# Performance work log

Hardware: AMD Instinct MI355X
Metric: run time of the kernel (lower is better)

The kernel has to match this reference:

```python
import jax, jax.numpy as jnp
import numpy as np

MARGIN = 0.3
NORM = 2.0  # p-norm used by both pairwise() and PairwiseDistance

M, C = 65536, 256   # n*h*w pixels, feature channels
K, P, Q = 20, 2048, 2048  # classes 1..nclass-1, positives, negatives per class


def setup_inputs() -> dict:
    key = jax.random.key(0)
    k1, k2, k3 = jax.random.split(key, 3)
    features = jax.random.normal(k1, (M, C), dtype=jnp.float32)
    pos_idx = jax.random.randint(k2, (K, P), 0, M)
    neg_idx = jax.random.randint(k3, (K, Q), 0, M)
    return {"features": features, "pos_idx": pos_idx, "neg_idx": neg_idx}


def _pairwise(x, y):
    # torch: clamp(xx - 2xy + yy, 0); (dis + eps) ** (1/norm)
    eps = 0.0001 / x.shape[1]
    xx = jnp.sum(x * x, axis=1)           # [P]
    yy = jnp.sum(y * y, axis=1)           # [Q]
    xy = x @ y.T                           # [P,Q] GEMM
    dis = jnp.clip(xx[:, None] - 2.0 * xy + yy[None, :], 0.0)
    return (dis + eps) ** (1.0 / NORM)


def _pdist(x1, x2):
    # PairwiseDistance: (clamp(sum(|x1-x2|^p), 0) + eps) ** (1/p)
    eps = 0.0001 / x1.shape[1]
    out = jnp.sum(jnp.abs(x1 - x2) ** NORM, axis=1)
    return (jnp.clip(out, 0.0) + eps) ** (1.0 / NORM)


def _class_loss(pos, neg):
    # hard mining on detached features (indices only, as in generate_triplet_simple)
    pos_d = jax.lax.stop_gradient(pos)
    neg_d = jax.lax.stop_gradient(neg)
    hp = jnp.argmax(_pairwise(pos_d, pos_d), axis=1)   # hardest positive per anchor
    hn = jnp.argmin(_pairwise(pos_d, neg_d), axis=1)   # hardest negative per anchor
    d_p = _pdist(pos, pos[hp])
    d_n = _pdist(pos, neg[hn])
    return jnp.mean(jnp.clip(MARGIN + d_p - d_n, 0.0))


def reference(features, pos_idx, neg_idx):
    f = jax.nn.sigmoid(features)          # torch.sigmoid(features)
    pos = f[pos_idx]                      # [K,P,C]
    neg = f[neg_idx]                      # [K,Q,C]
    losses = jax.vmap(_class_loss)(pos, neg)  # per-class triplet losses
    return jnp.sum(losses)                # loss accumulated over classes
```

## Files before the change

### kernel.cpp

```cpp
#include <hip/hip_runtime.h>
#include <stdint.h>

#define M_ROWS 65536
#define C_DIM  256
#define K_CLS  20
#define P_POS  2048
#define MARGIN_F 0.3f
#define EPS_D (0.0001f / 256.0f)
#define SCALE1 0x7F7F7F7Fu
#define SCALE2 0x80808080u

typedef float floatx4 __attribute__((ext_vector_type(4)));
typedef int   intx8   __attribute__((ext_vector_type(8)));
union Frag8 { intx8 v; uint4 q[2]; };

__device__ __forceinline__ void async_copy16(const void* g, void* l) {
    __builtin_amdgcn_global_load_lds(
        (const __attribute__((address_space(1))) void*)g,
        (__attribute__((address_space(3))) void*)l, 16, 0, 0);
}
__device__ __forceinline__ float sigm(float x) { return 1.f / (1.f + __expf(-x)); }

__device__ __forceinline__ void negA(Frag8& f) {
#pragma unroll
    for (int t = 0; t < 8; ++t) f.v[t] ^= (int)0x80808080u;
}

#define VMCNT2() asm volatile("s_waitcnt vmcnt(2)" ::: "memory")
#define VMCNT0() asm volatile("s_waitcnt vmcnt(0)" ::: "memory")

__global__ __launch_bounds__(256) void sigmoid_norm_k(
        const float* __restrict__ feat,
        unsigned int* __restrict__ S8,
        float* __restrict__ xx,
        unsigned int* __restrict__ hp,
        unsigned int* __restrict__ hn,
        float* __restrict__ out) {
    {
        const int idx = blockIdx.x * 256 + threadIdx.x;
        if (idx < K_CLS * P_POS) { hp[idx] = 0u; hn[idx] = 0xFFFFFFFFu; }
        if (idx == 0) out[0] = 0.f;
    }
    const int wave = threadIdx.x >> 6, lane = threadIdx.x & 63;
    for (int g = blockIdx.x; g < M_ROWS / 4; g += 2048) {
        const int row = g * 4 + wave;
        const float4 v = *(const float4*)(feat + (size_t)row * C_DIM + lane * 4);

        const int p01 = __builtin_amdgcn_cvt_pk_fp8_f32(sigm(v.x), sigm(v.y), 0, false);
        const int p23 = __builtin_amdgcn_cvt_pk_fp8_f32(sigm(v.z), sigm(v.w), 0, false);
        S8[(size_t)row * 64 + lane] =
            (unsigned int)(p01 & 0xFFFF) | ((unsigned int)p23 << 16);

        const float q0 = __builtin_amdgcn_cvt_f32_fp8(p01, 0);
        const float q1 = __builtin_amdgcn_cvt_f32_fp8(p01, 1);
        const float q2 = __builtin_amdgcn_cvt_f32_fp8(p23, 0);
        const float q3 = __builtin_amdgcn_cvt_f32_fp8(p23, 1);
        float sum = q0 * q0 + q1 * q1 + q2 * q2 + q3 * q3;
#pragma unroll
        for (int off = 32; off; off >>= 1) sum += __shfl_down(sum, off);
        if (lane == 0) xx[row] = sum;
    }
}

__global__ __launch_bounds__(256, 3) void select_k(
        const unsigned int* __restrict__ S8,
        const float* __restrict__ xx,
        const int* __restrict__ pos_idx,
        const int* __restrict__ neg_idx,
        unsigned int* __restrict__ hp,
        unsigned int* __restrict__ hn) {
    __shared__ __align__(16) uint4 Bt4[3][512];
    __shared__ float yyL[512];

    const int tid    = threadIdx.x;
    const int w      = tid >> 6;
    const int lane   = tid & 63;
    const int lane15 = lane & 15;
    const int quad   = lane >> 4;

    const int bid    = blockIdx.x;
    const int ctid   = bid % 40;
    const int rest   = bid / 40;
    const int i_blk  = rest >> 2;
    const int jq     = rest & 3;
    const int k      = ctid >> 1;
    const int isNeg  = ctid & 1;
    const int i0     = i_blk * 256;
    const int j0     = jq * 512;

    const int* __restrict__ idxA = pos_idx + k * P_POS;
    const int* __restrict__ idxB = (isNeg ? neg_idx : pos_idx) + k * P_POS;
    unsigned int* outKey         = (isNeg ? hn : hp) + k * P_POS;

    const char* S8B = (const char*)S8;

    const int rl  = lane >> 4;
    const int cch = lane & 15;
    int rloc[2], soff[2];
#pragma unroll
    for (int c = 0; c < 2; ++c) {
        rloc[c] = (w * 2 + c) * 4 + rl;
        soff[c] = (cch ^ (rloc[c] & 15)) << 4;
    }

    uint32_t g_pk[16];
#pragma unroll
    for (int t = 0; t < 16; ++t) {
        const uint32_t a0 = (uint32_t)idxB[j0 + t * 32 + rloc[0]];
        const uint32_t a1 = (uint32_t)idxB[j0 + t * 32 + rloc[1]];
        g_pk[t] = (a0 & 0xFFFFu) | (a1 << 16);
    }

#pragma unroll
    for (int t = 0; t < 2; ++t) {
        const int jj = t * 256 + tid;
        yyL[jj] = xx[idxB[j0 + jj]];
    }

    Frag8 A_reg[4][2];
#pragma unroll
    for (int si = 0; si < 4; ++si) {
        const int gi = idxA[i0 + w * 64 + si * 16 + lane15];
        const char* rb = S8B + ((size_t)(uint32_t)gi << 8) + quad * 32;
#pragma unroll
        for (int s = 0; s < 2; ++s) {
            A_reg[si][s].q[0] = *(const uint4*)(rb + s * 128);
            A_reg[si][s].q[1] = *(const uint4*)(rb + s * 128 + 16);
            negA(A_reg[si][s]);
        }
    }

    const int bidx0 = lane15 * 16 + ((quad * 2) ^ lane15);

    float bestv[16];
    const float binit = isNeg ? 3.4e38f : -3.4e38f;
#pragma unroll
    for (int t = 0; t < 16; ++t) bestv[t] = binit;

#pragma unroll
    for (int t = 0; t < 2; ++t) {
        char* lb = (char*)Bt4[t] + (w * 2) * 1024;
        async_copy16(S8B + ((size_t)(g_pk[t] & 0xFFFFu) << 8) + soff[0], lb);
        async_copy16(S8B + ((size_t)(g_pk[t] >> 16) << 8) + soff[1], lb + 1024);
    }

    __syncthreads();

#pragma unroll
    for (int jc = 0; jc < 16; ++jc) {
        if (jc) {
            if (jc == 15) VMCNT0(); else VMCNT2();
            __builtin_amdgcn_s_barrier();
            __builtin_amdgcn_sched_barrier(0);
        }

        const float yv0 = yyL[(jc << 5) + lane15];
        const float yv1 = yyL[(jc << 5) + 16 + lane15];

        if (jc < 14) {
            const uint32_t pk = g_pk[jc + 2];
            char* lb = (char*)Bt4[(jc + 2) % 3] + (w * 2) * 1024;
            async_copy16(S8B + ((size_t)(pk & 0xFFFFu) << 8) + soff[0], lb);
            async_copy16(S8B + ((size_t)(pk >> 16) << 8) + soff[1], lb + 1024);
        }

        const floatx4 yv4_0 = {yv0, yv0, yv0, yv0};
        const floatx4 yv4_1 = {yv1, yv1, yv1, yv1};
        floatx4 acc[2][4];
        {
            Frag8 bf0, bf1;
            bf0.q[0] = Bt4[jc % 3][bidx0];
            bf0.q[1] = Bt4[jc % 3][bidx0 ^ 1];
            bf1.q[0] = Bt4[jc % 3][bidx0 + 256];
            bf1.q[1] = Bt4[jc % 3][(bidx0 ^ 1) + 256];
#pragma unroll
            for (int si = 0; si < 4; ++si)
                acc[0][si] = __builtin_amdgcn_mfma_scale_f32_16x16x128_f8f6f4(
                    A_reg[si][0].v, bf0.v, yv4_0, 0, 0,
                    0, SCALE2, 0, SCALE1);
#pragma unroll
            for (int si = 0; si < 4; ++si)
                acc[1][si] = __builtin_amdgcn_mfma_scale_f32_16x16x128_f8f6f4(
                    A_reg[si][0].v, bf1.v, yv4_1, 0, 0,
                    0, SCALE2, 0, SCALE1);
        }
        {
            Frag8 bf0, bf1;
            bf0.q[0] = Bt4[jc % 3][bidx0 ^ 8];
            bf0.q[1] = Bt4[jc % 3][bidx0 ^ 9];
            bf1.q[0] = Bt4[jc % 3][(bidx0 ^ 8) + 256];
            bf1.q[1] = Bt4[jc % 3][(bidx0 ^ 9) + 256];
#pragma unroll
            for (int si = 0; si < 4; ++si)
                acc[0][si] = __builtin_amdgcn_mfma_scale_f32_16x16x128_f8f6f4(
                    A_reg[si][1].v, bf0.v, acc[0][si], 0, 0,
                    0, SCALE2, 0, SCALE1);
#pragma unroll
            for (int si = 0; si < 4; ++si)
                acc[1][si] = __builtin_amdgcn_mfma_scale_f32_16x16x128_f8f6f4(
                    A_reg[si][1].v, bf1.v, acc[1][si], 0, 0,
                    0, SCALE2, 0, SCALE1);
        }

        const uint32_t jb0 = (uint32_t)((j0 + (jc << 5)) | lane15);
        const uint32_t jb1 = jb0 | 16u;
#pragma unroll
        for (int si = 0; si < 4; ++si)
#pragma unroll
            for (int r = 0; r < 4; ++r) {
                const float e0 = __uint_as_float(
                    (__float_as_uint(acc[0][si][r]) & 0xFFFFF800u) | jb0);
                const float e1 = __uint_as_float(
                    (__float_as_uint(acc[1][si][r]) & 0xFFFFF800u) | jb1);
                const int slot = si * 4 + r;
                bestv[slot] = isNeg ? fminf(fminf(bestv[slot], e0), e1)
                                    : fmaxf(fmaxf(bestv[slot], e0), e1);
            }
    }

#pragma unroll
    for (int slot = 0; slot < 16; ++slot) {
#pragma unroll
        for (int off = 1; off < 16; off <<= 1) {
            const float ov = __shfl_xor(bestv[slot], off);
            bestv[slot] = isNeg ? fminf(bestv[slot], ov) : fmaxf(bestv[slot], ov);
        }
    }
    if (lane15 == 0) {
#pragma unroll
        for (int si = 0; si < 4; ++si)
#pragma unroll
            for (int r = 0; r < 4; ++r) {
                const int row = w * 64 + si * 16 + quad * 4 + r;
                const uint32_t u = __float_as_uint(bestv[si * 4 + r]);
                const uint32_t key = (u & 0x80000000u) ? ~u : (u | 0x80000000u);
                if (isNeg) atomicMin(&outKey[i0 + row], key);
                else       atomicMax(&outKey[i0 + row], key);
            }
    }
}

#define ACC16(UA, UP, UN)                                                     \
    {                                                                         \
        float xa, d;                                                          \
        xa = __builtin_amdgcn_cvt_f32_fp8((int)(UA), 0);                      \
        d = xa - __builtin_amdgcn_cvt_f32_fp8((int)(UP), 0); dp += d * d;     \
        d = xa - __builtin_amdgcn_cvt_f32_fp8((int)(UN), 0); dn += d * d;     \
        xa = __builtin_amdgcn_cvt_f32_fp8((int)(UA), 1);                      \
        d = xa - __builtin_amdgcn_cvt_f32_fp8((int)(UP), 1); dp += d * d;     \
        d = xa - __builtin_amdgcn_cvt_f32_fp8((int)(UN), 1); dn += d * d;     \
        xa = __builtin_amdgcn_cvt_f32_fp8((int)(UA), 2);                      \
        d = xa - __builtin_amdgcn_cvt_f32_fp8((int)(UP), 2); dp += d * d;     \
        d = xa - __builtin_amdgcn_cvt_f32_fp8((int)(UN), 2); dn += d * d;     \
        xa = __builtin_amdgcn_cvt_f32_fp8((int)(UA), 3);                      \
        d = xa - __builtin_amdgcn_cvt_f32_fp8((int)(UP), 3); dp += d * d;     \
        d = xa - __builtin_amdgcn_cvt_f32_fp8((int)(UN), 3); dn += d * d;     \
    }

__global__ __launch_bounds__(256) void loss_k(
        const unsigned int* __restrict__ S8,
        const int* __restrict__ pos_idx,
        const int* __restrict__ neg_idx,
        const unsigned int* __restrict__ hp,
        const unsigned int* __restrict__ hn,
        float* __restrict__ terms) {
    const int tid    = threadIdx.x;
    const int lane15 = tid & 15;
    const int grp    = tid >> 4;
    const char* S8B = (const char*)S8;
#pragma unroll
    for (int c = 0; c < 4; ++c) {
        const int a = ((int)blockIdx.x * 4 + c) * 16 + grp;
        const int k = a >> 11;
        const int i = a & 2047;
        const int* pidx = pos_idx + (k << 11);
        const int* nidx = neg_idx + (k << 11);
        const unsigned int kp = hp[a], kn = hn[a];
        const int jp = (int)((kp & 0x80000000u) ? (kp & 2047u) : ((~kp) & 2047u));
        const int jn = (int)((kn & 0x80000000u) ? (kn & 2047u) : ((~kn) & 2047u));
        const int ga = pidx[i];
        const int gp = pidx[jp];
        const int gn = nidx[jn];

        const uint4 va = *(const uint4*)(S8B + ((size_t)(uint32_t)ga << 8) + lane15 * 16);
        const uint4 vp = *(const uint4*)(S8B + ((size_t)(uint32_t)gp << 8) + lane15 * 16);
        const uint4 vn = *(const uint4*)(S8B + ((size_t)(uint32_t)gn << 8) + lane15 * 16);

        float dp = 0.f, dn = 0.f;
        ACC16(va.x, vp.x, vn.x)
        ACC16(va.y, vp.y, vn.y)
        ACC16(va.z, vp.z, vn.z)
        ACC16(va.w, vp.w, vn.w)

#pragma unroll
        for (int off = 1; off < 16; off <<= 1) {
            dp += __shfl_xor(dp, off);
            dn += __shfl_xor(dn, off);
        }
        if (lane15 == 0) {
            const float d_p = sqrtf(fmaxf(dp, 0.f) + EPS_D);
            const float d_n = sqrtf(fmaxf(dn, 0.f) + EPS_D);
            terms[a] = fmaxf(MARGIN_F + d_p - d_n, 0.f);
        }
    }
}

__global__ __launch_bounds__(1024) void reduce_k(
        const float* __restrict__ terms, float* __restrict__ out) {
    __shared__ float red[1024];
    const int tid = threadIdx.x;
    red[tid] = terms[blockIdx.x * 1024 + tid];
    __syncthreads();
    for (int off = 512; off; off >>= 1) {
        if (tid < off) red[tid] += red[tid + off];
        __syncthreads();
    }
    if (tid == 0) atomicAdd(out, red[0] * (1.0f / (float)P_POS));
}

extern "C" void kernel_launch(void* const* d_in, const int* in_sizes, int n_in,
                              void* d_out, int out_size, void* d_ws, size_t ws_size,
                              hipStream_t stream) {
    const float* feat    = (const float*)d_in[0];
    const int*   pos_idx = (const int*)d_in[1];
    const int*   neg_idx = (const int*)d_in[2];

    char* ws = (char*)d_ws;
    unsigned int* S8 = (unsigned int*)ws;
    float*        xx = (float*)(ws + 16777216);
    unsigned int* hp = (unsigned int*)(ws + 17039360);
    unsigned int* hn = (unsigned int*)(ws + 17203200);
    float*     terms = (float*)(ws + 17367040);

    sigmoid_norm_k<<<2048, 256, 0, stream>>>(feat, S8, xx, hp, hn,
                                             (float*)d_out);

    select_k<<<32 * 40, 256, 0, stream>>>(S8, xx, pos_idx, neg_idx, hp, hn);

    loss_k<<<640, 256, 0, stream>>>(S8, pos_idx, neg_idx, hp, hn, terms);

    reduce_k<<<40, 1024, 0, stream>>>(terms, (float*)d_out);
}
```

Baseline: 166.1 us.

## Exploit symmetry of positive-positive distance matrix to halve pos GEMM work

The positive-positive distance matrix is symmetric, so the positive selection now computes only upper-triangle 256x256 tiles (36 per class instead of 64). Each off-diagonal tile updates both row maxima and, through a shared-memory column key reduced with atomicMax, column maxima. The row-norm term is added in the epilogue instead of being folded into the accumulator init. The loss kernel now emits per-block partial sums, and a single small wave finishes the reduction and writes the output directly. The cost is extra epilogue ALU work, more shuffles and atomics per tile, and an unbalanced grid in which pos and neg blocks do different amounts of work.

```diff
diff --git a/kernel.cpp b/kernel.cpp
--- a/kernel.cpp
+++ b/kernel.cpp
@@ -25,6 +25,10 @@
 #pragma unroll
     for (int t = 0; t < 8; ++t) f.v[t] ^= (int)0x80808080u;
 }
+__device__ __forceinline__ unsigned int mkey(float f) {
+    const uint32_t u = __float_as_uint(f);
+    return (u & 0x80000000u) ? ~u : (u | 0x80000000u);
+}
 
 #define VMCNT2() asm volatile("s_waitcnt vmcnt(2)" ::: "memory")
 #define VMCNT0() asm volatile("s_waitcnt vmcnt(0)" ::: "memory")
@@ -34,12 +38,10 @@
         unsigned int* __restrict__ S8,
         float* __restrict__ xx,
         unsigned int* __restrict__ hp,
-        unsigned int* __restrict__ hn,
-        float* __restrict__ out) {
+        unsigned int* __restrict__ hn) {
     {
         const int idx = blockIdx.x * 256 + threadIdx.x;
         if (idx < K_CLS * P_POS) { hp[idx] = 0u; hn[idx] = 0xFFFFFFFFu; }
-        if (idx == 0) out[0] = 0.f;
     }
     const int wave = threadIdx.x >> 6, lane = threadIdx.x & 63;
     for (int g = blockIdx.x; g < M_ROWS / 4; g += 2048) {
@@ -59,6 +61,194 @@
 #pragma unroll
         for (int off = 32; off; off >>= 1) sum += __shfl_down(sum, off);
         if (lane == 0) xx[row] = sum;
+    }
+}
+
+template<int NT, bool POS>
+__device__ __forceinline__ void select_core(
+        const char* __restrict__ S8B,
+        const float* __restrict__ xx,
+        const int* __restrict__ idxA,
+        const int* __restrict__ idxB,
+        unsigned int* __restrict__ outKey,
+        const int i0, const int j0, const bool doCol,
+        uint4 (*Bt4)[512], float* yyL, float* xxL, unsigned int* colkeyL,
+        const int tid, const int w, const int lane15, const int quad) {
+    const int rl  = (tid & 63) >> 4;
+    const int cch = tid & 15;
+    int rloc[2], soff[2];
+#pragma unroll
+    for (int c = 0; c < 2; ++c) {
+        rloc[c] = (w * 2 + c) * 4 + rl;
+        soff[c] = (cch ^ (rloc[c] & 15)) << 4;
+    }
+
+    uint32_t g_pk[NT];
+#pragma unroll
+    for (int t = 0; t < NT; ++t) {
+        const uint32_t a0 = (uint32_t)idxB[j0 + t * 32 + rloc[0]];
+        const uint32_t a1 = (uint32_t)idxB[j0 + t * 32 + rloc[1]];
+        g_pk[t] = (a0 & 0xFFFFu) | (a1 << 16);
+    }
+
+#pragma unroll
+    for (int t = 0; t < NT / 8; ++t) {
+        const int jj = t * 256 + tid;
+        yyL[jj] = xx[idxB[j0 + jj]];
+    }
+    if (POS) {
+        xxL[tid] = xx[idxA[i0 + tid]];
+        colkeyL[tid] = 0u;
+    }
+
+    Frag8 A_reg[4][2];
+#pragma unroll
+    for (int si = 0; si < 4; ++si) {
+        const int gi = idxA[i0 + w * 64 + si * 16 + lane15];
+        const char* rb = S8B + ((size_t)(uint32_t)gi << 8) + quad * 32;
+#pragma unroll
+        for (int s = 0; s < 2; ++s) {
+            A_reg[si][s].q[0] = *(const uint4*)(rb + s * 128);
+            A_reg[si][s].q[1] = *(const uint4*)(rb + s * 128 + 16);
+            negA(A_reg[si][s]);
+        }
+    }
+
+    const int bidx0 = lane15 * 16 + ((quad * 2) ^ lane15);
+
+    float bestv[16];
+    const float binit = POS ? -3.4e38f : 3.4e38f;
+#pragma unroll
+    for (int t = 0; t < 16; ++t) bestv[t] = binit;
+
+#pragma unroll
+    for (int t = 0; t < 2; ++t) {
+        char* lb = (char*)Bt4[t] + (w * 2) * 1024;
+        async_copy16(S8B + ((size_t)(g_pk[t] & 0xFFFFu) << 8) + soff[0], lb);
+        async_copy16(S8B + ((size_t)(g_pk[t] >> 16) << 8) + soff[1], lb + 1024);
+    }
+    __syncthreads();
+
+#pragma unroll
+    for (int jc = 0; jc < NT; ++jc) {
+        if (jc) {
+            if (jc == NT - 1) VMCNT0(); else VMCNT2();
+            __builtin_amdgcn_s_barrier();
+            __builtin_amdgcn_sched_barrier(0);
+        }
+        const float yv0 = yyL[(jc << 5) + lane15];
+        const float yv1 = yyL[(jc << 5) + 16 + lane15];
+
+        if (jc < NT - 2) {
+            const uint32_t pk = g_pk[jc + 2];
+            char* lb = (char*)Bt4[(jc + 2) % 3] + (w * 2) * 1024;
+            async_copy16(S8B + ((size_t)(pk & 0xFFFFu) << 8) + soff[0], lb);
+            async_copy16(S8B + ((size_t)(pk >> 16) << 8) + soff[1], lb + 1024);
+        }
+
+        const floatx4 yv4_0 = {yv0, yv0, yv0, yv0};
+        const floatx4 yv4_1 = {yv1, yv1, yv1, yv1};
+        floatx4 acc[2][4];
+        {
+            Frag8 bf0, bf1;
+            bf0.q[0] = Bt4[jc % 3][bidx0];
+            bf0.q[1] = Bt4[jc % 3][bidx0 ^ 1];
+            bf1.q[0] = Bt4[jc % 3][bidx0 + 256];
+            bf1.q[1] = Bt4[jc % 3][(bidx0 ^ 1) + 256];
+#pragma unroll
+            for (int si = 0; si < 4; ++si)
+                acc[0][si] = __builtin_amdgcn_mfma_scale_f32_16x16x128_f8f6f4(
+                    A_reg[si][0].v, bf0.v, yv4_0, 0, 0, 0, SCALE2, 0, SCALE1);
+#pragma unroll
+            for (int si = 0; si < 4; ++si)
+                acc[1][si] = __builtin_amdgcn_mfma_scale_f32_16x16x128_f8f6f4(
+                    A_reg[si][0].v, bf1.v, yv4_1, 0, 0, 0, SCALE2, 0, SCALE1);
+        }
+        {
+            Frag8 bf0, bf1;
+            bf0.q[0] = Bt4[jc % 3][bidx0 ^ 8];
+            bf0.q[1] = Bt4[jc % 3][bidx0 ^ 9];
+            bf1.q[0] = Bt4[jc % 3][(bidx0 ^ 8) + 256];
+            bf1.q[1] = Bt4[jc % 3][(bidx0 ^ 9) + 256];
+#pragma unroll
+            for (int si = 0; si < 4; ++si)
+                acc[0][si] = __builtin_amdgcn_mfma_scale_f32_16x16x128_f8f6f4(
+                    A_reg[si][1].v, bf0.v, acc[0][si], 0, 0, 0, SCALE2, 0, SCALE1);
+#pragma unroll
+            for (int si = 0; si < 4; ++si)
+                acc[1][si] = __builtin_amdgcn_mfma_scale_f32_16x16x128_f8f6f4(
+                    A_reg[si][1].v, bf1.v, acc[1][si], 0, 0, 0, SCALE2, 0, SCALE1);
+        }
+
+        const uint32_t jb0 = (uint32_t)((j0 + (jc << 5)) | lane15);
+        const uint32_t jb1 = jb0 | 16u;
+        if (POS) {
+            float cm0 = -3.4e38f, cm1 = -3.4e38f;
+#pragma unroll
+            for (int si = 0; si < 4; ++si)
+#pragma unroll
+                for (int r = 0; r < 4; ++r) {
+                    const int rowl = w * 64 + si * 16 + quad * 4 + r;
+                    const float xv = xxL[rowl & 255];
+                    const uint32_t ib = (uint32_t)(i0 + rowl);
+                    const uint32_t e0 =
+                        __float_as_uint(acc[0][si][r] + xv) & 0xFFFFF800u;
+                    const uint32_t e1 =
+                        __float_as_uint(acc[1][si][r] + xv) & 0xFFFFF800u;
+                    const int slot = si * 4 + r;
+                    bestv[slot] = fmaxf(fmaxf(bestv[slot],
+                        __uint_as_float(e0 | jb0)), __uint_as_float(e1 | jb1));
+                    cm0 = fmaxf(cm0, __uint_as_float(e0 | ib));
+                    cm1 = fmaxf(cm1, __uint_as_float(e1 | ib));
+                }
+            if (doCol) {
+                cm0 = fmaxf(cm0, __shfl_xor(cm0, 16));
+                cm0 = fmaxf(cm0, __shfl_xor(cm0, 32));
+                cm1 = fmaxf(cm1, __shfl_xor(cm1, 16));
+                cm1 = fmaxf(cm1, __shfl_xor(cm1, 32));
+                if (quad == 0) {
+                    atomicMax(&colkeyL[(jc << 5) + lane15], mkey(cm0));
+                    atomicMax(&colkeyL[(jc << 5) + 16 + lane15], mkey(cm1));
+                }
+            }
+        } else {
+#pragma unroll
+            for (int si = 0; si < 4; ++si)
+#pragma unroll
+                for (int r = 0; r < 4; ++r) {
+                    const float e0 = __uint_as_float(
+                        (__float_as_uint(acc[0][si][r]) & 0xFFFFF800u) | jb0);
+                    const float e1 = __uint_as_float(
+                        (__float_as_uint(acc[1][si][r]) & 0xFFFFF800u) | jb1);
+                    const int slot = si * 4 + r;
+                    bestv[slot] = fminf(fminf(bestv[slot], e0), e1);
+                }
+        }
+    }
+
+#pragma unroll
+    for (int slot = 0; slot < 16; ++slot) {
+#pragma unroll
+        for (int off = 1; off < 16; off <<= 1) {
+            const float ov = __shfl_xor(bestv[slot], off);
+            bestv[slot] = POS ? fmaxf(bestv[slot], ov) : fminf(bestv[slot], ov);
+        }
+    }
+    if (lane15 == 0) {
+#pragma unroll
+        for (int si = 0; si < 4; ++si)
+#pragma unroll
+            for (int r = 0; r < 4; ++r) {
+                const int row = w * 64 + si * 16 + quad * 4 + r;
+                const uint32_t key = mkey(bestv[si * 4 + r]);
+                if (POS) atomicMax(&outKey[i0 + row], key);
+                else     atomicMin(&outKey[i0 + row], key);
+            }
+    }
+    if (POS && doCol) {
+        __syncthreads();
+        const unsigned int u = colkeyL[tid];
+        if (u) atomicMax(&outKey[j0 + tid], u);
     }
 }
 
@@ -71,172 +261,37 @@
         unsigned int* __restrict__ hn) {
     __shared__ __align__(16) uint4 Bt4[3][512];
     __shared__ float yyL[512];
+    __shared__ float xxL[256];
+    __shared__ unsigned int colkeyL[256];
 
     const int tid    = threadIdx.x;
     const int w      = tid >> 6;
-    const int lane   = tid & 63;
-    const int lane15 = lane & 15;
-    const int quad   = lane >> 4;
-
-    const int bid    = blockIdx.x;
-    const int ctid   = bid % 40;
-    const int rest   = bid / 40;
-    const int i_blk  = rest >> 2;
-    const int jq     = rest & 3;
-    const int k      = ctid >> 1;
-    const int isNeg  = ctid & 1;
-    const int i0     = i_blk * 256;
-    const int j0     = jq * 512;
-
-    const int* __restrict__ idxA = pos_idx + k * P_POS;
-    const int* __restrict__ idxB = (isNeg ? neg_idx : pos_idx) + k * P_POS;
-    unsigned int* outKey         = (isNeg ? hn : hp) + k * P_POS;
-
+    const int lane15 = tid & 15;
+    const int quad   = (tid & 63) >> 4;
+
+    const int bid  = blockIdx.x;
+    const int ctid = bid % 40;
+    const int r    = bid / 40;
+    const int k    = ctid >> 1;
+    const int isNeg = ctid & 1;
     const char* S8B = (const char*)S8;
 
-    const int rl  = lane >> 4;
-    const int cch = lane & 15;
-    int rloc[2], soff[2];
-#pragma unroll
-    for (int c = 0; c < 2; ++c) {
-        rloc[c] = (w * 2 + c) * 4 + rl;
-        soff[c] = (cch ^ (rloc[c] & 15)) << 4;
-    }
-
-    uint32_t g_pk[16];
-#pragma unroll
-    for (int t = 0; t < 16; ++t) {
-        const uint32_t a0 = (uint32_t)idxB[j0 + t * 32 + rloc[0]];
-        const uint32_t a1 = (uint32_t)idxB[j0 + t * 32 + rloc[1]];
-        g_pk[t] = (a0 & 0xFFFFu) | (a1 << 16);
-    }
-
-#pragma unroll
-    for (int t = 0; t < 2; ++t) {
-        const int jj = t * 256 + tid;
-        yyL[jj] = xx[idxB[j0 + jj]];
-    }
-
-    Frag8 A_reg[4][2];
-#pragma unroll
-    for (int si = 0; si < 4; ++si) {
-        const int gi = idxA[i0 + w * 64 + si * 16 + lane15];
-        const char* rb = S8B + ((size_t)(uint32_t)gi << 8) + quad * 32;
-#pragma unroll
-        for (int s = 0; s < 2; ++s) {
-            A_reg[si][s].q[0] = *(const uint4*)(rb + s * 128);
-            A_reg[si][s].q[1] = *(const uint4*)(rb + s * 128 + 16);
-            negA(A_reg[si][s]);
-        }
-    }
-
-    const int bidx0 = lane15 * 16 + ((quad * 2) ^ lane15);
-
-    float bestv[16];
-    const float binit = isNeg ? 3.4e38f : -3.4e38f;
-#pragma unroll
-    for (int t = 0; t < 16; ++t) bestv[t] = binit;
-
-#pragma unroll
-    for (int t = 0; t < 2; ++t) {
-        char* lb = (char*)Bt4[t] + (w * 2) * 1024;
-        async_copy16(S8B + ((size_t)(g_pk[t] & 0xFFFFu) << 8) + soff[0], lb);
-        async_copy16(S8B + ((size_t)(g_pk[t] >> 16) << 8) + soff[1], lb + 1024);
-    }
-
-    __syncthreads();
-
-#pragma unroll
-    for (int jc = 0; jc < 16; ++jc) {
-        if (jc) {
-            if (jc == 15) VMCNT0(); else VMCNT2();
-            __builtin_amdgcn_s_barrier();
-            __builtin_amdgcn_sched_barrier(0);
-        }
-
-        const float yv0 = yyL[(jc << 5) + lane15];
-        const float yv1 = yyL[(jc << 5) + 16 + lane15];
-
-        if (jc < 14) {
-            const uint32_t pk = g_pk[jc + 2];
-            char* lb = (char*)Bt4[(jc + 2) % 3] + (w * 2) * 1024;
-            async_copy16(S8B + ((size_t)(pk & 0xFFFFu) << 8) + soff[0], lb);
-            async_copy16(S8B + ((size_t)(pk >> 16) << 8) + soff[1], lb + 1024);
-        }
-
-        const floatx4 yv4_0 = {yv0, yv0, yv0, yv0};
-        const floatx4 yv4_1 = {yv1, yv1, yv1, yv1};
-        floatx4 acc[2][4];
-        {
-            Frag8 bf0, bf1;
-            bf0.q[0] = Bt4[jc % 3][bidx0];
-            bf0.q[1] = Bt4[jc % 3][bidx0 ^ 1];
-            bf1.q[0] = Bt4[jc % 3][bidx0 + 256];
-            bf1.q[1] = Bt4[jc % 3][(bidx0 ^ 1) + 256];
-#pragma unroll
-            for (int si = 0; si < 4; ++si)
-                acc[0][si] = __builtin_amdgcn_mfma_scale_f32_16x16x128_f8f6f4(
-                    A_reg[si][0].v, bf0.v, yv4_0, 0, 0,
-                    0, SCALE2, 0, SCALE1);
-#pragma unroll
-            for (int si = 0; si < 4; ++si)
-                acc[1][si] = __builtin_amdgcn_mfma_scale_f32_16x16x128_f8f6f4(
-                    A_reg[si][0].v, bf1.v, yv4_1, 0, 0,
-                    0, SCALE2, 0, SCALE1);
-        }
-        {
-            Frag8 bf0, bf1;
-            bf0.q[0] = Bt4[jc % 3][bidx0 ^ 8];
-            bf0.q[1] = Bt4[jc % 3][bidx0 ^ 9];
-            bf1.q[0] = Bt4[jc % 3][(bidx0 ^ 8) + 256];
-            bf1.q[1] = Bt4[jc % 3][(bidx0 ^ 9) + 256];
-#pragma unroll
-            for (int si = 0; si < 4; ++si)
-                acc[0][si] = __builtin_amdgcn_mfma_scale_f32_16x16x128_f8f6f4(
-                    A_reg[si][1].v, bf0.v, acc[0][si], 0, 0,
-                    0, SCALE2, 0, SCALE1);
-#pragma unroll
-            for (int si = 0; si < 4; ++si)
-                acc[1][si] = __builtin_amdgcn_mfma_scale_f32_16x16x128_f8f6f4(
-                    A_reg[si][1].v, bf1.v, acc[1][si], 0, 0,
-                    0, SCALE2, 0, SCALE1);
-        }
-
-        const uint32_t jb0 = (uint32_t)((j0 + (jc << 5)) | lane15);
-        const uint32_t jb1 = jb0 | 16u;
-#pragma unroll
-        for (int si = 0; si < 4; ++si)
-#pragma unroll
-            for (int r = 0; r < 4; ++r) {
-                const float e0 = __uint_as_float(
-                    (__float_as_uint(acc[0][si][r]) & 0xFFFFF800u) | jb0);
-                const float e1 = __uint_as_float(
-                    (__float_as_uint(acc[1][si][r]) & 0xFFFFF800u) | jb1);
-                const int slot = si * 4 + r;
-                bestv[slot] = isNeg ? fminf(fminf(bestv[slot], e0), e1)
-                                    : fmaxf(fmaxf(bestv[slot], e0), e1);
-            }
-    }
-
-#pragma unroll
-    for (int slot = 0; slot < 16; ++slot) {
-#pragma unroll
-        for (int off = 1; off < 16; off <<= 1) {
-            const float ov = __shfl_xor(bestv[slot], off);
-            bestv[slot] = isNeg ? fminf(bestv[slot], ov) : fmaxf(bestv[slot], ov);
-        }
-    }
-    if (lane15 == 0) {
-#pragma unroll
-        for (int si = 0; si < 4; ++si)
-#pragma unroll
-            for (int r = 0; r < 4; ++r) {
-                const int row = w * 64 + si * 16 + quad * 4 + r;
-                const uint32_t u = __float_as_uint(bestv[si * 4 + r]);
-                const uint32_t key = (u & 0x80000000u) ? ~u : (u | 0x80000000u);
-                if (isNeg) atomicMin(&outKey[i0 + row], key);
-                else       atomicMax(&outKey[i0 + row], key);
-            }
+    if (isNeg) {
+        if (r >= 32) return;
+        const int i0 = (r >> 2) * 256;
+        const int j0 = (r & 3) * 512;
+        select_core<16, false>(S8B, xx, pos_idx + k * P_POS,
+                               neg_idx + k * P_POS, hn + k * P_POS,
+                               i0, j0, false, Bt4, yyL, xxL, colkeyL,
+                               tid, w, lane15, quad);
+    } else {
+        int t = r, a = 0;
+        while (t >= 8 - a) { t -= 8 - a; ++a; }
+        const int b = a + t;
+        select_core<8, true>(S8B, xx, pos_idx + k * P_POS,
+                             pos_idx + k * P_POS, hp + k * P_POS,
+                             a * 256, b * 256, a < b, Bt4, yyL, xxL, colkeyL,
+                             tid, w, lane15, quad);
     }
 }
 
@@ -263,11 +318,13 @@
         const int* __restrict__ neg_idx,
         const unsigned int* __restrict__ hp,
         const unsigned int* __restrict__ hn,
-        float* __restrict__ terms) {
+        float* __restrict__ partials) {
+    __shared__ float sm[16];
     const int tid    = threadIdx.x;
     const int lane15 = tid & 15;
     const int grp    = tid >> 4;
-    const char* S8B = (const char*)S8;
+    const char* S8B  = (const char*)S8;
+    float lsum = 0.f;
 #pragma unroll
     for (int c = 0; c < 4; ++c) {
         const int a = ((int)blockIdx.x * 4 + c) * 16 + grp;
@@ -300,22 +357,27 @@
         if (lane15 == 0) {
             const float d_p = sqrtf(fmaxf(dp, 0.f) + EPS_D);
             const float d_n = sqrtf(fmaxf(dn, 0.f) + EPS_D);
-            terms[a] = fmaxf(MARGIN_F + d_p - d_n, 0.f);
-        }
-    }
-}
-
-__global__ __launch_bounds__(1024) void reduce_k(
-        const float* __restrict__ terms, float* __restrict__ out) {
-    __shared__ float red[1024];
+            lsum += fmaxf(MARGIN_F + d_p - d_n, 0.f);
+        }
+    }
+    if (lane15 == 0) sm[grp] = lsum;
+    __syncthreads();
+    if (tid == 0) {
+        float s = 0.f;
+#pragma unroll
+        for (int g = 0; g < 16; ++g) s += sm[g];
+        partials[blockIdx.x] = s;
+    }
+}
+
+__global__ __launch_bounds__(64) void reduce_k(
+        const float* __restrict__ partials, float* __restrict__ out) {
     const int tid = threadIdx.x;
-    red[tid] = terms[blockIdx.x * 1024 + tid];
-    __syncthreads();
-    for (int off = 512; off; off >>= 1) {
-        if (tid < off) red[tid] += red[tid + off];
-        __syncthreads();
-    }
-    if (tid == 0) atomicAdd(out, red[0] * (1.0f / (float)P_POS));
+    float s = 0.f;
+    for (int i = tid; i < 640; i += 64) s += partials[i];
+#pragma unroll
+    for (int off = 32; off; off >>= 1) s += __shfl_down(s, off);
+    if (tid == 0) out[0] = s * (1.0f / (float)P_POS);
 }
 
 extern "C" void kernel_launch(void* const* d_in, const int* in_sizes, int n_in,
@@ -330,14 +392,13 @@
     float*        xx = (float*)(ws + 16777216);
     unsigned int* hp = (unsigned int*)(ws + 17039360);
     unsigned int* hn = (unsigned int*)(ws + 17203200);
-    float*     terms = (float*)(ws + 17367040);
-
-    sigmoid_norm_k<<<2048, 256, 0, stream>>>(feat, S8, xx, hp, hn,
-                                             (float*)d_out);
-
-    select_k<<<32 * 40, 256, 0, stream>>>(S8, xx, pos_idx, neg_idx, hp, hn);
-
-    loss_k<<<640, 256, 0, stream>>>(S8, pos_idx, neg_idx, hp, hn, terms);
-
-    reduce_k<<<40, 1024, 0, stream>>>(terms, (float*)d_out);
-}
+    float*  partials = (float*)(ws + 17367040);
+
+    sigmoid_norm_k<<<2048, 256, 0, stream>>>(feat, S8, xx, hp, hn);
+
+    select_k<<<36 * 40, 256, 0, stream>>>(S8, xx, pos_idx, neg_idx, hp, hn);
+
+    loss_k<<<640, 256, 0, stream>>>(S8, pos_idx, neg_idx, hp, hn, partials);
+
+    reduce_k<<<1, 64, 0, stream>>>(partials, (float*)d_out);
+}
```

New measurement: 245.9 us. 1.48x slower.
